# Kernel tuning notes

Hardware: AMD Instinct MI355X
Metric: run time of the kernel (lower is better)

The kernel has to match this reference:

```python
import jax, jax.numpy as jnp
import numpy as np

NUM_HEADS = 16
LN_EPS = 1e-5


def setup_inputs() -> dict:
    key = jax.random.key(0)
    ks = jax.random.split(key, 7)
    B, S, D = 4, 1024, 1024
    s_in = 1.0 / np.sqrt(D)
    return {
        "x": jax.random.normal(ks[0], (B, S, D), dtype=jnp.float32),
        # PyTorch MHA packed in-projection: [3D, D] weight, [3D] bias
        "w_qkv": jax.random.uniform(ks[1], (3 * D, D), dtype=jnp.float32, minval=-s_in, maxval=s_in),
        "b_qkv": jnp.zeros((3 * D,), dtype=jnp.float32),
        "w_out": jax.random.uniform(ks[2], (D, D), dtype=jnp.float32, minval=-s_in, maxval=s_in),
        "b_out": jnp.zeros((D,), dtype=jnp.float32),
        "ln_w": jnp.ones((D,), dtype=jnp.float32),
        "ln_b": jnp.zeros((D,), dtype=jnp.float32),
    }


def _layernorm(x, w, b):
    m = jnp.mean(x, axis=-1, keepdims=True)
    v = jnp.var(x, axis=-1, keepdims=True)
    return (x - m) * jax.lax.rsqrt(v + LN_EPS) * w + b


def reference(x, w_qkv, b_qkv, w_out, b_out, ln_w, ln_b):
    B, S, D = x.shape
    H = NUM_HEADS
    hd = D // H
    # packed QKV projection (torch: F.linear(x, w_qkv, b_qkv) then chunk)
    qkv = x @ w_qkv.T + b_qkv                      # [B, S, 3D]
    q, k, v = jnp.split(qkv, 3, axis=-1)
    q = q.reshape(B, S, H, hd).transpose(0, 2, 1, 3) * (hd ** -0.5)  # [B,H,S,hd]
    k = k.reshape(B, S, H, hd).transpose(0, 2, 1, 3)
    v = v.reshape(B, S, H, hd).transpose(0, 2, 1, 3)
    scores = jnp.einsum('bhqd,bhkd->bhqk', q, k)   # [B,H,S,S]
    attn = jax.nn.softmax(scores, axis=-1)
    ctx = jnp.einsum('bhqk,bhkd->bhqd', attn, v)   # [B,H,S,hd]
    ctx = ctx.transpose(0, 2, 1, 3).reshape(B, S, D)
    attn_out = ctx @ w_out.T + b_out
    # torch returns head-averaged weights (average_attn_weights=True)
    attn_weights = attn.mean(axis=1)               # [B,S,S]
    # dropout rate 0.0 -> identity; residual + LayerNorm
    y = _layernorm(x + attn_out, ln_w, ln_b)
    return y, attn_weights
```

## Files before the change

kernel.cpp:

```cpp
#include <hip/hip_runtime.h>
#include <cstdint>

typedef __bf16 bf16;
typedef __bf16 bf16x8 __attribute__((ext_vector_type(8)));
typedef __bf16 bf16x4 __attribute__((ext_vector_type(4)));
typedef float  f32x4  __attribute__((ext_vector_type(4)));

#define MFMA_BF16(a, b, c) __builtin_amdgcn_mfma_f32_16x16x32_bf16(a, b, c, 0, 0, 0)

__device__ __forceinline__ void async_load16(const void* g, void* l) {
    __builtin_amdgcn_global_load_lds(
        (__attribute__((address_space(1))) uint32_t*)(uintptr_t)g,
        (__attribute__((address_space(3))) uint32_t*)(uint32_t)(uintptr_t)l,
        16, 0, 0);
}

__global__ void cvt_kernel(const float* __restrict__ src, bf16* __restrict__ dst, int n4) {
    int i = blockIdx.x * blockDim.x + threadIdx.x;
    if (i < n4) {
        float4 v = ((const float4*)src)[i];
        bf16x4 o;
        o[0] = (bf16)v.x; o[1] = (bf16)v.y; o[2] = (bf16)v.z; o[3] = (bf16)v.w;
        ((bf16x4*)dst)[i] = o;
    }
}

__global__ __launch_bounds__(256) void gemm_qkv_kernel(
    const bf16* __restrict__ A, const bf16* __restrict__ W,
    const float* __restrict__ bias,
    bf16* __restrict__ Qb, bf16* __restrict__ Kb, bf16* __restrict__ Vt)
{
    const int Kd = 1024;
    __shared__ bf16 sA[128 * 32];
    __shared__ bf16 sB[128 * 32];
    int tid = threadIdx.x, lane = tid & 63, wid = tid >> 6;
    int m0 = blockIdx.y * 128, n0 = blockIdx.x * 128;
    int srow = wid * 32 + (lane >> 2);
    int scol = (lane & 3) * 8;
    const bf16* Ag = A + (size_t)(m0 + srow) * Kd + scol;
    const bf16* Wg = W + (size_t)(n0 + srow) * Kd + scol;
    bf16* sAp = &sA[srow * 32 + scol];
    bf16* sBp = &sB[srow * 32 + scol];
    int wm = (wid & 1) * 64, wn = (wid >> 1) * 64;
    int lcol = lane & 15, quad = lane >> 4;
    f32x4 acc[4][4] = {};
    for (int k0 = 0; k0 < Kd; k0 += 32) {
        __syncthreads();
        async_load16(Ag + k0, sAp);
        async_load16(Ag + k0 + 16 * Kd, sAp + 16 * 32);
        async_load16(Wg + k0, sBp);
        async_load16(Wg + k0 + 16 * Kd, sBp + 16 * 32);
        __syncthreads();
        bf16x8 af[4], bfr[4];
#pragma unroll
        for (int i = 0; i < 4; i++)
            af[i] = *(const bf16x8*)&sA[(wm + i * 16 + lcol) * 32 + quad * 8];
#pragma unroll
        for (int i = 0; i < 4; i++)
            bfr[i] = *(const bf16x8*)&sB[(wn + i * 16 + lcol) * 32 + quad * 8];
#pragma unroll
        for (int i = 0; i < 4; i++)
#pragma unroll
            for (int j = 0; j < 4; j++)
                acc[i][j] = MFMA_BF16(af[i], bfr[j], acc[i][j]);
    }
#pragma unroll
    for (int j = 0; j < 4; j++) {
        int n = n0 + wn + j * 16 + lcol;
        float bv = bias[n];
        int part = n >> 10, d = n & 1023, h = d >> 6, dd = d & 63;
#pragma unroll
        for (int i = 0; i < 4; i++) {
            int mb = m0 + wm + i * 16 + quad * 4;
            int b = mb >> 10, s = mb & 1023;
            if (part == 2) {
                bf16x4 v4;
#pragma unroll
                for (int r = 0; r < 4; r++) v4[r] = (bf16)(acc[i][j][r] + bv);
                *(bf16x4*)&Vt[(size_t)((b * 16 + h) * 64 + dd) * 1024 + s] = v4;
            } else {
                float scv = (part == 0) ? 0.125f : 1.0f;
                bf16* dst = (part == 0 ? Qb : Kb) + (size_t)((b * 16 + h) * 1024 + s) * 64 + dd;
#pragma unroll
                for (int r = 0; r < 4; r++) dst[(size_t)r * 64] = (bf16)((acc[i][j][r] + bv) * scv);
            }
        }
    }
}

__global__ __launch_bounds__(256) void gemm_out_kernel(
    const bf16* __restrict__ A, const bf16* __restrict__ W,
    const float* __restrict__ bias, float* __restrict__ out)
{
    const int Kd = 1024;
    __shared__ bf16 sA[128 * 32];
    __shared__ bf16 sB[128 * 32];
    int tid = threadIdx.x, lane = tid & 63, wid = tid >> 6;
    int m0 = blockIdx.y * 128, n0 = blockIdx.x * 128;
    int srow = wid * 32 + (lane >> 2);
    int scol = (lane & 3) * 8;
    const bf16* Ag = A + (size_t)(m0 + srow) * Kd + scol;
    const bf16* Wg = W + (size_t)(n0 + srow) * Kd + scol;
    bf16* sAp = &sA[srow * 32 + scol];
    bf16* sBp = &sB[srow * 32 + scol];
    int wm = (wid & 1) * 64, wn = (wid >> 1) * 64;
    int lcol = lane & 15, quad = lane >> 4;
    f32x4 acc[4][4] = {};
    for (int k0 = 0; k0 < Kd; k0 += 32) {
        __syncthreads();
        async_load16(Ag + k0, sAp);
        async_load16(Ag + k0 + 16 * Kd, sAp + 16 * 32);
        async_load16(Wg + k0, sBp);
        async_load16(Wg + k0 + 16 * Kd, sBp + 16 * 32);
        __syncthreads();
        bf16x8 af[4], bfr[4];
#pragma unroll
        for (int i = 0; i < 4; i++)
            af[i] = *(const bf16x8*)&sA[(wm + i * 16 + lcol) * 32 + quad * 8];
#pragma unroll
        for (int i = 0; i < 4; i++)
            bfr[i] = *(const bf16x8*)&sB[(wn + i * 16 + lcol) * 32 + quad * 8];
#pragma unroll
        for (int i = 0; i < 4; i++)
#pragma unroll
            for (int j = 0; j < 4; j++)
                acc[i][j] = MFMA_BF16(af[i], bfr[j], acc[i][j]);
    }
#pragma unroll
    for (int j = 0; j < 4; j++) {
        int n = n0 + wn + j * 16 + lcol;
        float bv = bias[n];
#pragma unroll
        for (int i = 0; i < 4; i++) {
            int m = m0 + wm + i * 16 + quad * 4;
#pragma unroll
            for (int r = 0; r < 4; r++) out[(size_t)(m + r) * 1024 + n] = acc[i][j][r] + bv;
        }
    }
}

#define PTS 72
__global__ __launch_bounds__(256) void flash_kernel(
    const bf16* __restrict__ Qb, const bf16* __restrict__ Kb, const bf16* __restrict__ Vt,
    bf16* __restrict__ ctx, float* __restrict__ ml)
{
    __shared__ bf16 sK[64 * 64];
    __shared__ bf16 sV[64 * 64];
    __shared__ bf16 pt[4 * 16 * PTS];
    int tid = threadIdx.x, lane = tid & 63, wid = tid >> 6;
    int bx = blockIdx.x;
    int qt = bx & 15;
    int h = (bx >> 4) & 15;
    int b = bx >> 8;
    int lcol = lane & 15, quad = lane >> 4;
    size_t base = (size_t)(b * 16 + h) * 65536;

    int q0 = qt * 64 + wid * 16;
    const bf16* qp = Qb + base + (size_t)(q0 + lcol) * 64 + quad * 8;
    bf16x8 a0 = *(const bf16x8*)qp;
    bf16x8 a1 = *(const bf16x8*)(qp + 32);

    bf16* wp = pt + wid * 16 * PTS;
    int rr8 = lane >> 3;
    int pp  = lane & 7;
    int jj  = pp ^ rr8;
    int sr0 = wid * 16 + rr8;
    int sw  = lcol & 7;

    float l_[4] = {0.f, 0.f, 0.f, 0.f};
    f32x4 o[4] = {};

    for (int kt = 0; kt < 16; kt++) {
        __syncthreads();
        async_load16(Kb + base + (size_t)(kt * 64 + sr0) * 64 + jj * 8,       &sK[sr0 * 64 + pp * 8]);
        async_load16(Kb + base + (size_t)(kt * 64 + sr0 + 8) * 64 + jj * 8,   &sK[(sr0 + 8) * 64 + pp * 8]);
        async_load16(Vt + base + (size_t)sr0 * 1024 + kt * 64 + jj * 8,       &sV[sr0 * 64 + pp * 8]);
        async_load16(Vt + base + (size_t)(sr0 + 8) * 1024 + kt * 64 + jj * 8, &sV[(sr0 + 8) * 64 + pp * 8]);
        __syncthreads();
#pragma unroll
        for (int nt = 0; nt < 4; nt++) {
            int ck = quad ^ sw;
            bf16x8 bk0 = *(const bf16x8*)&sK[(nt * 16 + lcol) * 64 + ck * 8];
            bf16x8 bk1 = *(const bf16x8*)&sK[(nt * 16 + lcol) * 64 + (ck ^ 4) * 8];
            f32x4 s = {};
            s = MFMA_BF16(a0, bk0, s);
            s = MFMA_BF16(a1, bk1, s);
#pragma unroll
            for (int rr = 0; rr < 4; rr++) {
                float p = __expf(s[rr]);
                l_[rr] += p;
                wp[(quad * 4 + rr) * PTS + nt * 16 + lcol] = (bf16)p;
            }
        }
#pragma unroll
        for (int kf = 0; kf < 2; kf++) {
            bf16x8 pa = *(const bf16x8*)&wp[lcol * PTS + kf * 32 + quad * 8];
#pragma unroll
            for (int dt = 0; dt < 4; dt++) {
                bf16x8 vb = *(const bf16x8*)&sV[(dt * 16 + lcol) * 64 + ((kf * 4 + quad) ^ sw) * 8];
                o[dt] = MFMA_BF16(pa, vb, o[dt]);
            }
        }
    }
#pragma unroll
    for (int mk = 1; mk < 16; mk <<= 1)
#pragma unroll
        for (int rr = 0; rr < 4; rr++) l_[rr] += __shfl_xor(l_[rr], mk, 64);
#pragma unroll
    for (int rr = 0; rr < 4; rr++) {
        float inv = 1.f / l_[rr];
        int qg = q0 + quad * 4 + rr;
#pragma unroll
        for (int dt = 0; dt < 4; dt++)
            ctx[(size_t)(b * 1024 + qg) * 1024 + h * 64 + dt * 16 + lcol] = (bf16)(o[dt][rr] * inv);
        if (lcol == 0)
            ml[(size_t)(b * 16 + h) * 1024 + qg] = l_[rr];
    }
}

__global__ __launch_bounds__(256) void aw_kernel(
    const bf16* __restrict__ Qb, const bf16* __restrict__ Kb,
    const float* __restrict__ ml, float* __restrict__ aw)
{
    __shared__ bf16 sK[64 * 64];
    int tid = threadIdx.x, lane = tid & 63, wid = tid >> 6;
    int bx = blockIdx.x;
    int kt = bx & 15;
    int qt = (bx >> 4) & 15;
    int b = bx >> 8;
    int lcol = lane & 15, quad = lane >> 4;
    int q0 = qt * 64 + wid * 16;
    int kbase = kt * 64;
    int sw = lcol & 7;
    float acc[16];
#pragma unroll
    for (int i = 0; i < 16; i++) acc[i] = 0.f;

    for (int h = 0; h < 16; h++) {
        size_t base = (size_t)(b * 16 + h) * 65536;
        __syncthreads();
#pragma unroll
        for (int i = 0; i < 2; i++) {
            int ci = tid + 256 * i;
            int r_ = ci >> 3;
            int pp = ci & 7;
            int jj = pp ^ (r_ & 7);
            async_load16(Kb + base + (size_t)(kbase + r_) * 64 + jj * 8, &sK[(size_t)ci * 8]);
        }
        const bf16* qp = Qb + base + (size_t)(q0 + lcol) * 64 + quad * 8;
        bf16x8 a0 = *(const bf16x8*)qp;
        bf16x8 a1 = *(const bf16x8*)(qp + 32);
        float scale[4];
#pragma unroll
        for (int rr = 0; rr < 4; rr++)
            scale[rr] = 0.0625f / ml[(size_t)(b * 16 + h) * 1024 + q0 + quad * 4 + rr];
        __syncthreads();
#pragma unroll
        for (int nt = 0; nt < 4; nt++) {
            int ck = quad ^ sw;
            bf16x8 bk0 = *(const bf16x8*)&sK[(nt * 16 + lcol) * 64 + ck * 8];
            bf16x8 bk1 = *(const bf16x8*)&sK[(nt * 16 + lcol) * 64 + (ck ^ 4) * 8];
            f32x4 s = {};
            s = MFMA_BF16(a0, bk0, s);
            s = MFMA_BF16(a1, bk1, s);
#pragma unroll
            for (int rr = 0; rr < 4; rr++)
                acc[nt * 4 + rr] += __expf(s[rr]) * scale[rr];
        }
    }
#pragma unroll
    for (int nt = 0; nt < 4; nt++)
#pragma unroll
        for (int rr = 0; rr < 4; rr++)
            aw[(size_t)(b * 1024 + q0 + quad * 4 + rr) * 1024 + kbase + nt * 16 + lcol] = acc[nt * 4 + rr];
}

__global__ __launch_bounds__(256) void ln_kernel(
    const float* __restrict__ x, const float* __restrict__ ao,
    const float* __restrict__ w, const float* __restrict__ bsh,
    float* __restrict__ y)
{
    int row = blockIdx.x, tid = threadIdx.x;
    float4 xv = ((const float4*)(x + (size_t)row * 1024))[tid];
    float4 av = ((const float4*)(ao + (size_t)row * 1024))[tid];
    float4 v = {xv.x + av.x, xv.y + av.y, xv.z + av.z, xv.w + av.w};
    float s = v.x + v.y + v.z + v.w;
    float ss = v.x * v.x + v.y * v.y + v.z * v.z + v.w * v.w;
#pragma unroll
    for (int off = 32; off; off >>= 1) { s += __shfl_down(s, off); ss += __shfl_down(ss, off); }
    __shared__ float rs[4], rss[4];
    int lane = tid & 63, wid = tid >> 6;
    if (lane == 0) { rs[wid] = s; rss[wid] = ss; }
    __syncthreads();
    s = rs[0] + rs[1] + rs[2] + rs[3];
    ss = rss[0] + rss[1] + rss[2] + rss[3];
    float mean = s * (1.f / 1024.f);
    float var = ss * (1.f / 1024.f) - mean * mean;
    float inv = rsqrtf(var + 1e-5f);
    float4 wv = ((const float4*)w)[tid];
    float4 bv = ((const float4*)bsh)[tid];
    float4 o;
    o.x = (v.x - mean) * inv * wv.x + bv.x;
    o.y = (v.y - mean) * inv * wv.y + bv.y;
    o.z = (v.z - mean) * inv * wv.z + bv.z;
    o.w = (v.w - mean) * inv * wv.w + bv.w;
    ((float4*)y)[row * 256 + tid] = o;
}

extern "C" void kernel_launch(void* const* d_in, const int* in_sizes, int n_in,
                              void* d_out, int out_size, void* d_ws, size_t ws_size,
                              hipStream_t stream) {
    const float* x     = (const float*)d_in[0];
    const float* w_qkv = (const float*)d_in[1];
    const float* b_qkv = (const float*)d_in[2];
    const float* w_out = (const float*)d_in[3];
    const float* b_out = (const float*)d_in[4];
    const float* ln_w  = (const float*)d_in[5];
    const float* ln_b  = (const float*)d_in[6];

    char* ws = (char*)d_ws;
    bf16*   Qb    = (bf16*)(ws);
    bf16*   Kb    = (bf16*)(ws + (8ull  << 20));
    bf16*   Vt    = (bf16*)(ws + (16ull << 20));
    bf16*   ctx   = (bf16*)(ws + (24ull << 20));
    float*  ml    = (float*)(ws + (32ull << 20));
    bf16*   x_bf  = (bf16*)(ws + (33ull << 20));
    bf16*   wq_bf = (bf16*)(ws + (41ull << 20));
    bf16*   wo_bf = (bf16*)(ws + (16ull << 20));
    float*  ao    = (float*)(ws);

    float* y_out  = (float*)d_out;
    float* aw_out = y_out + 4ull * 1024 * 1024;

    cvt_kernel<<<4096, 256, 0, stream>>>(x, x_bf, 1048576);
    cvt_kernel<<<3072, 256, 0, stream>>>(w_qkv, wq_bf, 786432);
    gemm_qkv_kernel<<<dim3(24, 32), 256, 0, stream>>>(x_bf, wq_bf, b_qkv, Qb, Kb, Vt);
    flash_kernel<<<1024, 256, 0, stream>>>(Qb, Kb, Vt, ctx, ml);
    aw_kernel<<<1024, 256, 0, stream>>>(Qb, Kb, ml, aw_out);
    cvt_kernel<<<1024, 256, 0, stream>>>(w_out, wo_bf, 262144);
    gemm_out_kernel<<<dim3(8, 32), 256, 0, stream>>>(ctx, wo_bf, b_out, ao);
    ln_kernel<<<4096, 256, 0, stream>>>(x, ao, ln_w, ln_b, y_out);
}
```

Baseline: 223.9 us.

## Double-buffer LDS tiles in GEMM, flash and attn-weight kernels; swizzle P buffer

Each of the output-projection GEMM, flash attention and head-averaged weight kernels now keeps two shared-memory stages. The next tile's global-to-LDS async loads are issued right after the barrier, before the current tile is computed, and the second barrier per iteration is removed. The aim is to overlap memory latency with MFMA work. Separately, the per-wave P scratch in the flash kernel drops its padded stride for an XOR-swizzled layout, to avoid LDS bank conflicts without the padding. The costs are doubled LDS use, which may lower occupancy, and a reliance on the barrier waiting for the earlier async loads to land.

```diff
diff --git a/kernel.cpp b/kernel.cpp
--- a/kernel.cpp
+++ b/kernel.cpp
@@ -93,38 +93,44 @@
     const float* __restrict__ bias, float* __restrict__ out)
 {
     const int Kd = 1024;
-    __shared__ bf16 sA[128 * 32];
-    __shared__ bf16 sB[128 * 32];
+    __shared__ bf16 sA[2][128 * 32];
+    __shared__ bf16 sB[2][128 * 32];
     int tid = threadIdx.x, lane = tid & 63, wid = tid >> 6;
     int m0 = blockIdx.y * 128, n0 = blockIdx.x * 128;
     int srow = wid * 32 + (lane >> 2);
     int scol = (lane & 3) * 8;
     const bf16* Ag = A + (size_t)(m0 + srow) * Kd + scol;
     const bf16* Wg = W + (size_t)(n0 + srow) * Kd + scol;
-    bf16* sAp = &sA[srow * 32 + scol];
-    bf16* sBp = &sB[srow * 32 + scol];
+    int soff = srow * 32 + scol;
     int wm = (wid & 1) * 64, wn = (wid >> 1) * 64;
     int lcol = lane & 15, quad = lane >> 4;
     f32x4 acc[4][4] = {};
+    async_load16(Ag, &sA[0][soff]);
+    async_load16(Ag + 16 * Kd, &sA[0][soff + 512]);
+    async_load16(Wg, &sB[0][soff]);
+    async_load16(Wg + 16 * Kd, &sB[0][soff + 512]);
+    int cur = 0;
     for (int k0 = 0; k0 < Kd; k0 += 32) {
         __syncthreads();
-        async_load16(Ag + k0, sAp);
-        async_load16(Ag + k0 + 16 * Kd, sAp + 16 * 32);
-        async_load16(Wg + k0, sBp);
-        async_load16(Wg + k0 + 16 * Kd, sBp + 16 * 32);
-        __syncthreads();
+        if (k0 + 32 < Kd) {
+            async_load16(Ag + k0 + 32, &sA[cur ^ 1][soff]);
+            async_load16(Ag + k0 + 32 + 16 * Kd, &sA[cur ^ 1][soff + 512]);
+            async_load16(Wg + k0 + 32, &sB[cur ^ 1][soff]);
+            async_load16(Wg + k0 + 32 + 16 * Kd, &sB[cur ^ 1][soff + 512]);
+        }
         bf16x8 af[4], bfr[4];
 #pragma unroll
         for (int i = 0; i < 4; i++)
-            af[i] = *(const bf16x8*)&sA[(wm + i * 16 + lcol) * 32 + quad * 8];
-#pragma unroll
-        for (int i = 0; i < 4; i++)
-            bfr[i] = *(const bf16x8*)&sB[(wn + i * 16 + lcol) * 32 + quad * 8];
+            af[i] = *(const bf16x8*)&sA[cur][(wm + i * 16 + lcol) * 32 + quad * 8];
+#pragma unroll
+        for (int i = 0; i < 4; i++)
+            bfr[i] = *(const bf16x8*)&sB[cur][(wn + i * 16 + lcol) * 32 + quad * 8];
 #pragma unroll
         for (int i = 0; i < 4; i++)
 #pragma unroll
             for (int j = 0; j < 4; j++)
                 acc[i][j] = MFMA_BF16(af[i], bfr[j], acc[i][j]);
+        cur ^= 1;
     }
 #pragma unroll
     for (int j = 0; j < 4; j++) {
@@ -139,14 +145,13 @@
     }
 }
 
-#define PTS 72
 __global__ __launch_bounds__(256) void flash_kernel(
     const bf16* __restrict__ Qb, const bf16* __restrict__ Kb, const bf16* __restrict__ Vt,
     bf16* __restrict__ ctx, float* __restrict__ ml)
 {
-    __shared__ bf16 sK[64 * 64];
-    __shared__ bf16 sV[64 * 64];
-    __shared__ bf16 pt[4 * 16 * PTS];
+    __shared__ bf16 sK[2][64 * 64];
+    __shared__ bf16 sV[2][64 * 64];
+    __shared__ bf16 pt[4][16 * 64];
     int tid = threadIdx.x, lane = tid & 63, wid = tid >> 6;
     int bx = blockIdx.x;
     int qt = bx & 15;
@@ -160,28 +165,35 @@
     bf16x8 a0 = *(const bf16x8*)qp;
     bf16x8 a1 = *(const bf16x8*)(qp + 32);
 
-    bf16* wp = pt + wid * 16 * PTS;
+    char* wpt = (char*)&pt[wid][0];
     int rr8 = lane >> 3;
     int pp  = lane & 7;
     int jj  = pp ^ rr8;
     int sr0 = wid * 16 + rr8;
     int sw  = lcol & 7;
 
+#define STAGE_KV(buf, kt_) do { \
+        async_load16(Kb + base + (size_t)((kt_) * 64 + sr0) * 64 + jj * 8,       &sK[buf][sr0 * 64 + pp * 8]); \
+        async_load16(Kb + base + (size_t)((kt_) * 64 + sr0 + 8) * 64 + jj * 8,   &sK[buf][(sr0 + 8) * 64 + pp * 8]); \
+        async_load16(Vt + base + (size_t)sr0 * 1024 + (kt_) * 64 + jj * 8,       &sV[buf][sr0 * 64 + pp * 8]); \
+        async_load16(Vt + base + (size_t)(sr0 + 8) * 1024 + (kt_) * 64 + jj * 8, &sV[buf][(sr0 + 8) * 64 + pp * 8]); \
+    } while (0)
+
     float l_[4] = {0.f, 0.f, 0.f, 0.f};
     f32x4 o[4] = {};
 
+    STAGE_KV(0, 0);
+    int cur = 0;
     for (int kt = 0; kt < 16; kt++) {
         __syncthreads();
-        async_load16(Kb + base + (size_t)(kt * 64 + sr0) * 64 + jj * 8,       &sK[sr0 * 64 + pp * 8]);
-        async_load16(Kb + base + (size_t)(kt * 64 + sr0 + 8) * 64 + jj * 8,   &sK[(sr0 + 8) * 64 + pp * 8]);
-        async_load16(Vt + base + (size_t)sr0 * 1024 + kt * 64 + jj * 8,       &sV[sr0 * 64 + pp * 8]);
-        async_load16(Vt + base + (size_t)(sr0 + 8) * 1024 + kt * 64 + jj * 8, &sV[(sr0 + 8) * 64 + pp * 8]);
-        __syncthreads();
+        if (kt < 15) STAGE_KV(cur ^ 1, kt + 1);
+        const bf16* sKc = &sK[cur][0];
+        const bf16* sVc = &sV[cur][0];
 #pragma unroll
         for (int nt = 0; nt < 4; nt++) {
             int ck = quad ^ sw;
-            bf16x8 bk0 = *(const bf16x8*)&sK[(nt * 16 + lcol) * 64 + ck * 8];
-            bf16x8 bk1 = *(const bf16x8*)&sK[(nt * 16 + lcol) * 64 + (ck ^ 4) * 8];
+            bf16x8 bk0 = *(const bf16x8*)&sKc[(nt * 16 + lcol) * 64 + ck * 8];
+            bf16x8 bk1 = *(const bf16x8*)&sKc[(nt * 16 + lcol) * 64 + (ck ^ 4) * 8];
             f32x4 s = {};
             s = MFMA_BF16(a0, bk0, s);
             s = MFMA_BF16(a1, bk1, s);
@@ -189,19 +201,22 @@
             for (int rr = 0; rr < 4; rr++) {
                 float p = __expf(s[rr]);
                 l_[rr] += p;
-                wp[(quad * 4 + rr) * PTS + nt * 16 + lcol] = (bf16)p;
+                int row = quad * 4 + rr;
+                *(bf16*)(wpt + row * 128 + ((nt * 32 + lcol * 2) ^ ((row & 7) << 4))) = (bf16)p;
             }
         }
 #pragma unroll
         for (int kf = 0; kf < 2; kf++) {
-            bf16x8 pa = *(const bf16x8*)&wp[lcol * PTS + kf * 32 + quad * 8];
+            bf16x8 pa = *(const bf16x8*)(wpt + lcol * 128 + (((kf * 4 + quad) ^ sw) << 4));
 #pragma unroll
             for (int dt = 0; dt < 4; dt++) {
-                bf16x8 vb = *(const bf16x8*)&sV[(dt * 16 + lcol) * 64 + ((kf * 4 + quad) ^ sw) * 8];
+                bf16x8 vb = *(const bf16x8*)&sVc[(dt * 16 + lcol) * 64 + ((kf * 4 + quad) ^ sw) * 8];
                 o[dt] = MFMA_BF16(pa, vb, o[dt]);
             }
         }
-    }
+        cur ^= 1;
+    }
+#undef STAGE_KV
 #pragma unroll
     for (int mk = 1; mk < 16; mk <<= 1)
 #pragma unroll
@@ -222,7 +237,7 @@
     const bf16* __restrict__ Qb, const bf16* __restrict__ Kb,
     const float* __restrict__ ml, float* __restrict__ aw)
 {
-    __shared__ bf16 sK[64 * 64];
+    __shared__ bf16 sK[2][64 * 64];
     int tid = threadIdx.x, lane = tid & 63, wid = tid >> 6;
     int bx = blockIdx.x;
     int kt = bx & 15;
@@ -232,21 +247,23 @@
     int q0 = qt * 64 + wid * 16;
     int kbase = kt * 64;
     int sw = lcol & 7;
+    int r0_ = tid >> 3, p0_ = tid & 7, j0_ = p0_ ^ (r0_ & 7);
+    int r1_ = (tid + 256) >> 3, p1_ = (tid + 256) & 7, j1_ = p1_ ^ (r1_ & 7);
+
+#define STAGE_K(buf, hh) do { \
+        size_t hb_ = (size_t)(b * 16 + (hh)) * 65536; \
+        async_load16(Kb + hb_ + (size_t)(kbase + r0_) * 64 + j0_ * 8, &sK[buf][(size_t)tid * 8]); \
+        async_load16(Kb + hb_ + (size_t)(kbase + r1_) * 64 + j1_ * 8, &sK[buf][(size_t)(tid + 256) * 8]); \
+    } while (0)
+
     float acc[16];
 #pragma unroll
     for (int i = 0; i < 16; i++) acc[i] = 0.f;
 
+    STAGE_K(0, 0);
+    int cur = 0;
     for (int h = 0; h < 16; h++) {
         size_t base = (size_t)(b * 16 + h) * 65536;
-        __syncthreads();
-#pragma unroll
-        for (int i = 0; i < 2; i++) {
-            int ci = tid + 256 * i;
-            int r_ = ci >> 3;
-            int pp = ci & 7;
-            int jj = pp ^ (r_ & 7);
-            async_load16(Kb + base + (size_t)(kbase + r_) * 64 + jj * 8, &sK[(size_t)ci * 8]);
-        }
         const bf16* qp = Qb + base + (size_t)(q0 + lcol) * 64 + quad * 8;
         bf16x8 a0 = *(const bf16x8*)qp;
         bf16x8 a1 = *(const bf16x8*)(qp + 32);
@@ -255,11 +272,12 @@
         for (int rr = 0; rr < 4; rr++)
             scale[rr] = 0.0625f / ml[(size_t)(b * 16 + h) * 1024 + q0 + quad * 4 + rr];
         __syncthreads();
+        if (h < 15) STAGE_K(cur ^ 1, h + 1);
 #pragma unroll
         for (int nt = 0; nt < 4; nt++) {
             int ck = quad ^ sw;
-            bf16x8 bk0 = *(const bf16x8*)&sK[(nt * 16 + lcol) * 64 + ck * 8];
-            bf16x8 bk1 = *(const bf16x8*)&sK[(nt * 16 + lcol) * 64 + (ck ^ 4) * 8];
+            bf16x8 bk0 = *(const bf16x8*)&sK[cur][(nt * 16 + lcol) * 64 + ck * 8];
+            bf16x8 bk1 = *(const bf16x8*)&sK[cur][(nt * 16 + lcol) * 64 + (ck ^ 4) * 8];
             f32x4 s = {};
             s = MFMA_BF16(a0, bk0, s);
             s = MFMA_BF16(a1, bk1, s);
@@ -267,7 +285,9 @@
             for (int rr = 0; rr < 4; rr++)
                 acc[nt * 4 + rr] += __expf(s[rr]) * scale[rr];
         }
-    }
+        cur ^= 1;
+    }
+#undef STAGE_K
 #pragma unroll
     for (int nt = 0; nt < 4; nt++)
 #pragma unroll
```

Measured after the change: 220.2 us. About the same (-1.7%).
